# Performance work log

Hardware: AMD Instinct MI355X
Metric: run time of the kernel (lower is better)

The kernel has to match this reference:

```python
import jax, jax.numpy as jnp
import numpy as np

B, T, C = 2, 2048, 1024
H = 16
D = C // H          # head_dim = 64
WIN = 256           # local window


def _rope(x):
    # x: [B, H, T, D]; rotate pairs (even, odd) with per-pair frequencies.
    t = x.shape[2]
    d = x.shape[-1] // 2
    theta = 10000.0 ** (-(jnp.arange(d, dtype=x.dtype) / d))          # [d]
    ang = jnp.arange(t, dtype=x.dtype)[:, None] * theta               # [T, d]
    sin, cos = jnp.sin(ang), jnp.cos(ang)                             # [T, d]
    x1, x2 = x[..., ::2], x[..., 1::2]                                # [B,H,T,d]
    out = jnp.stack([x1 * cos - x2 * sin, x1 * sin + x2 * cos], axis=-1)
    return out.reshape(x.shape)


def setup_inputs() -> dict:
    key = jax.random.key(0)
    k1, k2, k3 = jax.random.split(key, 3)
    s = 1.0 / np.sqrt(C)
    return {
        "x": jax.random.normal(k1, (B, T, C), dtype=jnp.float32),
        "w_qkv": jax.random.normal(k2, (3 * C, C), dtype=jnp.float32) * s,
        "w_out": jax.random.normal(k3, (C, C), dtype=jnp.float32) * s,
        "b_out": jnp.zeros((C,), dtype=jnp.float32),
    }


def reference(x, w_qkv, w_out, b_out):
    b, t, c = x.shape
    qkv = x @ w_qkv.T                                   # [B,T,3C]
    qkv = qkv.reshape(b, t, H, 3 * D).transpose(0, 2, 1, 3)  # [B,H,T,3D]
    q, k, v = jnp.split(qkv, 3, axis=-1)                # each [B,H,T,D]
    q, k = _rope(q), _rope(k)
    scores = jnp.einsum("bhqd,bhkd->bhqk", q, k) / jnp.sqrt(jnp.asarray(D, x.dtype))
    i = jnp.arange(t)[:, None]
    j = jnp.arange(t)[None, :]
    mask = (j <= i) & (j >= i - WIN)                    # causal local window
    scores = jnp.where(mask, scores, -jnp.inf)
    attn = jax.nn.softmax(scores, axis=-1)              # [B,H,T,T]
    out = jnp.einsum("bhqk,bhkd->bhqd", attn, v)        # [B,H,T,D]
    out = out.transpose(0, 2, 1, 3).reshape(b, t, c)    # [B,T,C]
    return out @ w_out.T + b_out
```

## Files before the change

### kernel.cpp

```cpp
#include <hip/hip_runtime.h>
#include <math.h>

#define BB 2
#define TT 2048
#define CC 1024
#define HH 16
#define DD 64
#define WINW 256

constexpr int MROWS  = BB * TT;
constexpr int NQKV   = 3 * CC;
constexpr int QKV_LD = 3 * CC;

typedef unsigned short ushort_t;
typedef __attribute__((ext_vector_type(8))) short  bf16x8;
typedef __attribute__((ext_vector_type(4))) float  f32x4;
typedef __attribute__((ext_vector_type(8))) unsigned short u16x8;

__device__ __forceinline__ float bf2f(ushort_t u) {
    return __uint_as_float(((unsigned int)u) << 16);
}
__device__ __forceinline__ ushort_t f2bf(float f) {
    unsigned int u = __float_as_uint(f);
    u += 0x7fffu + ((u >> 16) & 1u);
    return (ushort_t)(u >> 16);
}

__device__ __forceinline__ void async16(void* lds, const void* g) {
    __builtin_amdgcn_global_load_lds(
        (const __attribute__((address_space(1))) unsigned int*)g,
        (__attribute__((address_space(3))) unsigned int*)lds, 16, 0, 0);
}

#define ROPE_LN 0.2878231366242557f

constexpr int NX = MROWS * CC;
constexpr int NQ = NQKV * CC;
constexpr int NO = CC * CC;

__global__ __launch_bounds__(256)
void convert_all(const float* __restrict__ x, const float* __restrict__ wq,
                 const float* __restrict__ wo, ushort_t* __restrict__ xb,
                 ushort_t* __restrict__ wqb, ushort_t* __restrict__ wob) {
    int i = (blockIdx.x * 256 + threadIdx.x) * 4;
    const float* src;
    ushort_t* dst;
    if (i < NX)           { src = x  + i;             dst = xb  + i; }
    else if (i < NX + NQ) { src = wq + (i - NX);      dst = wqb + (i - NX); }
    else                  { src = wo + (i - NX - NQ); dst = wob + (i - NX - NQ); }
    float4 v = *(const float4*)src;
    ushort4 o;
    o.x = f2bf(v.x); o.y = f2bf(v.y); o.z = f2bf(v.z); o.w = f2bf(v.w);
    *(ushort4*)dst = o;
}

__global__ __launch_bounds__(512)
void gemm1_8phase(const ushort_t* __restrict__ A, const ushort_t* __restrict__ Bw,
                  ushort_t* __restrict__ Cc) {
    constexpr int K = 1024, N = 3072, NT = 16;
    __shared__ __align__(16) ushort_t As[2][2][256 * 32];
    __shared__ __align__(16) ushort_t Bs[2][2][256 * 32];

    const int tid  = threadIdx.x;
    const int lane = tid & 63;
    const int w    = tid >> 6;
    const int wm   = w >> 2;
    const int wn   = w & 3;
    const int fr   = lane & 15;
    const int fq   = lane >> 4;

    const int nbx = NQKV / 256;
    int flat = blockIdx.y * nbx + blockIdx.x;
    flat = (flat & 7) * 24 + (flat >> 3);
    const int bm = (flat / nbx) * 256;
    const int bn = (flat % nbx) * 256;

    const int sr  = tid >> 2;
    const int dcb = tid & 3;
    const int scb = dcb ^ ((sr >> 1) & 3);

    const int cbr = fq ^ ((fr >> 1) & 3);

    f32x4 acc[8][4];
#pragma unroll
    for (int m = 0; m < 8; ++m)
#pragma unroll
        for (int n = 0; n < 4; ++n)
            acc[m][n] = f32x4{0.f, 0.f, 0.f, 0.f};

#pragma unroll
    for (int p = 0; p < 4; ++p) {
        const int skh = p >> 1;
        const bool isB = p & 1;
        const ushort_t* G = isB ? Bw : A;
        const int br = isB ? bn : bm;
        ushort_t* L = isB ? &Bs[0][skh][0] : &As[0][skh][0];
#pragma unroll
        for (int hh = 0; hh < 2; ++hh)
            async16(&L[(hh * 128 + sr) * 32 + dcb * 8],
                    G + (size_t)(br + hh * 128 + sr) * K + skh * 32 + scb * 8);
    }

    for (int t = 0; t < NT; ++t) {
        const int d  = t & 1;
        const int tn = (t + 1) & (NT - 1);
        bf16x8 bfr[4];

#pragma unroll
        for (int ph = 0; ph < 4; ++ph) {
            const int kh = ph >> 1;
            const int mh = ph & 1;

            {
                const int skh = ph >> 1;
                const bool isB = ph & 1;
                const ushort_t* G = isB ? Bw : A;
                const int br = isB ? bn : bm;
                ushort_t* L = isB ? &Bs[d ^ 1][skh][0] : &As[d ^ 1][skh][0];
#pragma unroll
                for (int hh = 0; hh < 2; ++hh)
                    async16(&L[(hh * 128 + sr) * 32 + dcb * 8],
                            G + (size_t)(br + hh * 128 + sr) * K
                              + (size_t)tn * 64 + skh * 32 + scb * 8);
            }

            if (mh == 0)
                asm volatile("s_waitcnt vmcnt(6)" ::: "memory");
            __builtin_amdgcn_s_barrier();
            __builtin_amdgcn_sched_barrier(0);

            if (mh == 0) {
#pragma unroll
                for (int n = 0; n < 4; ++n) {
                    const int rb = wn * 64 + n * 16 + fr;
                    bfr[n] = *(const bf16x8*)&Bs[d][kh][rb * 32 + cbr * 8];
                }
            }
            bf16x8 afr[4];
#pragma unroll
            for (int i = 0; i < 4; ++i) {
                const int ra = wm * 128 + (mh * 4 + i) * 16 + fr;
                afr[i] = *(const bf16x8*)&As[d][kh][ra * 32 + cbr * 8];
            }

            __builtin_amdgcn_s_setprio(1);
#pragma unroll
            for (int i = 0; i < 4; ++i)
#pragma unroll
                for (int n = 0; n < 4; ++n)
                    acc[mh * 4 + i][n] = __builtin_amdgcn_mfma_f32_16x16x32_bf16(
                        afr[i], bfr[n], acc[mh * 4 + i][n], 0, 0, 0);
            __builtin_amdgcn_s_setprio(0);
            __builtin_amdgcn_s_barrier();
        }
    }

    asm volatile("s_waitcnt vmcnt(0)" ::: "memory");

#pragma unroll
    for (int m = 0; m < 8; ++m)
#pragma unroll
        for (int n = 0; n < 4; ++n)
#pragma unroll
            for (int j = 0; j < 4; ++j) {
                const int row = bm + wm * 128 + m * 16 + fq * 4 + j;
                const int col = bn + wn * 64 + n * 16 + fr;
                Cc[(size_t)row * N + col] = f2bf(acc[m][n][j]);
            }
}

template <bool BIAS, bool OUT_BF16>
__global__ __launch_bounds__(256)
void gemm_nt_mfma(const ushort_t* __restrict__ A, const ushort_t* __restrict__ Bw,
                  const float* __restrict__ bias, void* __restrict__ Cc,
                  int M, int N, int K) {
    __shared__ __align__(16) ushort_t As[128 * 32];
    __shared__ __align__(16) ushort_t Bs[128 * 32];

    const int tid  = threadIdx.x;
    const int lane = tid & 63;
    const int wv   = tid >> 6;
    const int wr   = wv >> 1;
    const int wc   = wv & 1;

    const int nbx = gridDim.x;
    const int nwg = nbx * gridDim.y;
    int flat = blockIdx.y * nbx + blockIdx.x;
    flat = (flat & 7) * (nwg >> 3) + (flat >> 3);
    const int bm = (flat / nbx) * 128;
    const int bn = (flat % nbx) * 128;

    const int srow = tid >> 2;
    const int scol = (tid & 3) * 8;

    const ushort_t* Ag = A + (size_t)(bm + srow) * K + scol;
    const ushort_t* Bg = Bw + (size_t)(bn + srow) * K + scol;

    f32x4 acc[4][4];
#pragma unroll
    for (int m = 0; m < 4; ++m)
#pragma unroll
        for (int n = 0; n < 4; ++n)
            acc[m][n] = f32x4{0.f, 0.f, 0.f, 0.f};

    const int fr = lane & 15;
    const int fq = lane >> 4;

    for (int k0 = 0; k0 < K; k0 += 32) {
        async16(&As[tid * 8],        Ag);
        async16(&As[2048 + tid * 8], Ag + (size_t)64 * K);
        async16(&Bs[tid * 8],        Bg);
        async16(&Bs[2048 + tid * 8], Bg + (size_t)64 * K);
        Ag += 32; Bg += 32;
        __syncthreads();

        bf16x8 af[4], bfv[4];
#pragma unroll
        for (int m = 0; m < 4; ++m)
            af[m] = *(const bf16x8*)&As[(wr * 64 + m * 16 + fr) * 32 + fq * 8];
#pragma unroll
        for (int n = 0; n < 4; ++n)
            bfv[n] = *(const bf16x8*)&Bs[(wc * 64 + n * 16 + fr) * 32 + fq * 8];
#pragma unroll
        for (int m = 0; m < 4; ++m)
#pragma unroll
            for (int n = 0; n < 4; ++n)
                acc[m][n] = __builtin_amdgcn_mfma_f32_16x16x32_bf16(
                    af[m], bfv[n], acc[m][n], 0, 0, 0);
        __syncthreads();
    }

#pragma unroll
    for (int m = 0; m < 4; ++m) {
#pragma unroll
        for (int n = 0; n < 4; ++n) {
            const int col = bn + wc * 64 + n * 16 + fr;
            const float bv = BIAS ? bias[col] : 0.0f;
#pragma unroll
            for (int j = 0; j < 4; ++j) {
                const int row = bm + wr * 64 + m * 16 + fq * 4 + j;
                float v = acc[m][n][j] + bv;
                if (OUT_BF16)
                    ((ushort_t*)Cc)[(size_t)row * N + col] = f2bf(v);
                else
                    ((float*)Cc)[(size_t)row * N + col] = v;
            }
        }
    }
}

#define MASKNEG (-1e30f)

__global__ __launch_bounds__(512)
void attn_mfma(const ushort_t* __restrict__ qkv, ushort_t* __restrict__ out) {
    __shared__ __align__(16) ushort_t Ks[2][64 * 64];
    __shared__ __align__(16) ushort_t Vt[2][64 * 74];
    __shared__ __align__(16) ushort_t Ps[8][16 * 72];

    const int tid  = threadIdx.x;
    const int lane = tid & 63;
    const int w    = tid >> 6;
    const int fr   = lane & 15;
    const int fq   = lane >> 4;

    const int blk = blockIdx.x;
    const int qt  = blk & 15;
    const int h   = (blk >> 4) & 15;
    const int b   = blk >> 8;
    const int q0  = qt * 128;

    const ushort_t* base = qkv + (size_t)(b * TT) * QKV_LD + h * (3 * DD);

    const int srow = tid >> 3;
    const int dcb  = tid & 7;
    const int cbs  = dcb ^ (srow & 7);

    float thK[4];
#pragma unroll
    for (int e = 0; e < 4; ++e)
        thK[e] = __expf(-ROPE_LN * (float)(cbs * 4 + e));

    bf16x8 qf0, qf1;
    {
        const int tq = q0 + w * 16 + fr;
        const ushort_t* qrow = base + (size_t)tq * QKV_LD;
        u16x8 r0 = *(const u16x8*)(qrow + fq * 8);
        u16x8 r1 = *(const u16x8*)(qrow + 32 + fq * 8);
        const float tf = (float)tq;
#pragma unroll
        for (int e = 0; e < 4; ++e) {
            float th0 = __expf(-ROPE_LN * (float)(fq * 4 + e));
            float a0 = tf * th0;
            float s0 = __sinf(a0), c0 = __cosf(a0);
            float x1 = bf2f(r0[2 * e]), x2 = bf2f(r0[2 * e + 1]);
            r0[2 * e]     = f2bf(x1 * c0 - x2 * s0);
            r0[2 * e + 1] = f2bf(x1 * s0 + x2 * c0);
            float th1 = __expf(-ROPE_LN * (float)(16 + fq * 4 + e));
            float a1 = tf * th1;
            float s1 = __sinf(a1), c1 = __cosf(a1);
            float y1 = bf2f(r1[2 * e]), y2 = bf2f(r1[2 * e + 1]);
            r1[2 * e]     = f2bf(y1 * c1 - y2 * s1);
            r1[2 * e + 1] = f2bf(y1 * s1 + y2 * c1);
        }
        qf0 = *(bf16x8*)&r0;
        qf1 = *(bf16x8*)&r1;
    }

    f32x4 oacc[4];
#pragma unroll
    for (int nd = 0; nd < 4; ++nd) oacc[nd] = f32x4{0.f, 0.f, 0.f, 0.f};
    float mj[4], lj[4];
#pragma unroll
    for (int j = 0; j < 4; ++j) { mj[j] = MASKNEG; lj[j] = 0.f; }

    const int kstart = (q0 >= WINW) ? (q0 - WINW) : 0;
    const int ntiles = (q0 + 128 - kstart) >> 6;
    const int qlo = q0 + w * 16;

    {
        const ushort_t* rowp = base + (size_t)(kstart + srow) * QKV_LD;
        u16x8 kv = *(const u16x8*)(rowp + DD + cbs * 8);
        u16x8 vv = *(const u16x8*)(rowp + 2 * DD + dcb * 8);
        const float tf = (float)(kstart + srow);
#pragma unroll
        for (int e = 0; e < 4; ++e) {
            float a = tf * thK[e];
            float s = __sinf(a), c = __cosf(a);
            float x1 = bf2f(kv[2 * e]), x2 = bf2f(kv[2 * e + 1]);
            kv[2 * e]     = f2bf(x1 * c - x2 * s);
            kv[2 * e + 1] = f2bf(x1 * s + x2 * c);
        }
        *(u16x8*)&Ks[0][tid * 8] = kv;
#pragma unroll
        for (int e = 0; e < 8; ++e)
            Vt[0][(dcb * 8 + e) * 74 + srow] = vv[e];
    }
    __syncthreads();

    int cur = 0;
    for (int t = 0; t < ntiles; ++t) {
        const int kt0 = kstart + t * 64;
        const bool pf = (t + 1 < ntiles);
        const bool act = (kt0 <= qlo + 15) && (kt0 + 63 >= qlo - WINW);

        u16x8 kpre, vpre;
        if (pf) {
            const ushort_t* rowp = base + (size_t)(kt0 + 64 + srow) * QKV_LD;
            kpre = *(const u16x8*)(rowp + DD + cbs * 8);
            vpre = *(const u16x8*)(rowp + 2 * DD + dcb * 8);
        }

        if (act) {
            f32x4 s[4];
#pragma unroll
            for (int n = 0; n < 4; ++n) {
                const int krow = n * 16 + fr;
                bf16x8 kb0 = *(const bf16x8*)&Ks[cur][krow * 64 + ((fq ^ (krow & 7)) * 8)];
                bf16x8 kb1 = *(const bf16x8*)&Ks[cur][krow * 64 + (((fq + 4) ^ (krow & 7)) * 8)];
                f32x4 z = f32x4{0.f, 0.f, 0.f, 0.f};
                z = __builtin_amdgcn_mfma_f32_16x16x32_bf16(qf0, kb0, z, 0, 0, 0);
                s[n] = __builtin_amdgcn_mfma_f32_16x16x32_bf16(qf1, kb1, z, 0, 0, 0);
            }

            float pmax[4];
#pragma unroll
            for (int j = 0; j < 4; ++j) pmax[j] = MASKNEG;
#pragma unroll
            for (int n = 0; n < 4; ++n) {
                const int key = kt0 + n * 16 + fr;
#pragma unroll
                for (int j = 0; j < 4; ++j) {
                    const int qi = qlo + fq * 4 + j;
                    const bool ok = (key <= qi) && (key >= qi - WINW);
                    float sv = ok ? s[n][j] * 0.125f : MASKNEG;
                    s[n][j] = sv;
                    pmax[j] = fmaxf(pmax[j], sv);
                }
            }
#pragma unroll
            for (int off = 1; off < 16; off <<= 1)
#pragma unroll
                for (int j = 0; j < 4; ++j)
                    pmax[j] = fmaxf(pmax[j], __shfl_xor(pmax[j], off));

            float tl[4] = {0.f, 0.f, 0.f, 0.f};
#pragma unroll
            for (int j = 0; j < 4; ++j) {
                float mnew = fmaxf(mj[j], pmax[j]);
                float alpha = (mnew <= -1e29f) ? 1.0f : __expf(mj[j] - mnew);
                mj[j] = mnew;
                lj[j] *= alpha;
#pragma unroll
                for (int nd = 0; nd < 4; ++nd) oacc[nd][j] *= alpha;
            }
#pragma unroll
            for (int n = 0; n < 4; ++n) {
#pragma unroll
                for (int j = 0; j < 4; ++j) {
                    float sv = s[n][j];
                    float p = (sv <= -1e29f) ? 0.f : __expf(sv - mj[j]);
                    tl[j] += p;
                    Ps[w][(fq * 4 + j) * 72 + n * 16 + fr] = f2bf(p);
                }
            }
#pragma unroll
            for (int off = 1; off < 16; off <<= 1)
#pragma unroll
                for (int j = 0; j < 4; ++j)
                    tl[j] += __shfl_xor(tl[j], off);
#pragma unroll
            for (int j = 0; j < 4; ++j) lj[j] += tl[j];
        }

        if (pf) {
            const float tf = (float)(kt0 + 64 + srow);
#pragma unroll
            for (int e = 0; e < 4; ++e) {
                float a = tf * thK[e];
                float s2 = __sinf(a), c2 = __cosf(a);
                float x1 = bf2f(kpre[2 * e]), x2 = bf2f(kpre[2 * e + 1]);
                kpre[2 * e]     = f2bf(x1 * c2 - x2 * s2);
                kpre[2 * e + 1] = f2bf(x1 * s2 + x2 * c2);
            }
            *(u16x8*)&Ks[cur ^ 1][tid * 8] = kpre;
#pragma unroll
            for (int e = 0; e < 8; ++e)
                Vt[cur ^ 1][(dcb * 8 + e) * 74 + srow] = vpre[e];
        }

        if (act) {
            bf16x8 pa0 = *(const bf16x8*)&Ps[w][fr * 72 + fq * 8];
            bf16x8 pa1 = *(const bf16x8*)&Ps[w][fr * 72 + 32 + fq * 8];
#pragma unroll
            for (int nd = 0; nd < 4; ++nd) {
                bf16x8 vb0 = *(const bf16x8*)&Vt[cur][(nd * 16 + fr) * 74 + fq * 8];
                bf16x8 vb1 = *(const bf16x8*)&Vt[cur][(nd * 16 + fr) * 74 + 32 + fq * 8];
                oacc[nd] = __builtin_amdgcn_mfma_f32_16x16x32_bf16(pa0, vb0, oacc[nd], 0, 0, 0);
                oacc[nd] = __builtin_amdgcn_mfma_f32_16x16x32_bf16(pa1, vb1, oacc[nd], 0, 0, 0);
            }
        }

        __syncthreads();
        cur ^= 1;
    }

#pragma unroll
    for (int nd = 0; nd < 4; ++nd) {
#pragma unroll
        for (int j = 0; j < 4; ++j) {
            const int qi = qlo + fq * 4 + j;
            out[(size_t)(b * TT + qi) * CC + h * DD + nd * 16 + fr] =
                f2bf(oacc[nd][j] / lj[j]);
        }
    }
}

extern "C" void kernel_launch(void* const* d_in, const int* in_sizes, int n_in,
                              void* d_out, int out_size, void* d_ws, size_t ws_size,
                              hipStream_t stream) {
    const float* x     = (const float*)d_in[0];
    const float* w_qkv = (const float*)d_in[1];
    const float* w_out = (const float*)d_in[2];
    const float* b_out = (const float*)d_in[3];
    float* out = (float*)d_out;

    ushort_t* qkv_b  = (ushort_t*)d_ws;
    ushort_t* attn_b = qkv_b  + (size_t)MROWS * NQKV;
    ushort_t* xb     = attn_b + (size_t)MROWS * CC;
    ushort_t* wqb    = xb     + (size_t)MROWS * CC;
    ushort_t* wob    = wqb    + (size_t)NQKV * CC;

    convert_all<<<(NX + NQ + NO) / 1024, 256, 0, stream>>>(
        x, w_qkv, w_out, xb, wqb, wob);

    gemm1_8phase<<<dim3(NQKV / 256, MROWS / 256), 512, 0, stream>>>(
        xb, wqb, qkv_b);

    attn_mfma<<<BB * HH * (TT / 128), 512, 0, stream>>>(qkv_b, attn_b);

    gemm_nt_mfma<true, false><<<dim3(CC / 128, MROWS / 128), 256, 0, stream>>>(
        attn_b, wob, b_out, out, MROWS, CC, CC);
}
```

Before: 104.0 us.

## Use 256x192 tiles in QKV GEMM to fill all CUs

Shrinks the QKV projection GEMM's N tile from 256 to 192 columns, raising the grid from 12x16=192 to 16x16=256 workgroups so it matches the 256 CUs on MI355X and avoids a partial wave. The B tile layout becomes a single 192x64 LDS buffer with an 8-way XOR swizzle, and the async load schedule and vmcnt wait are reworked to match. Each block does less work per A load, so data reuse per tile drops a little.

```diff
diff --git a/kernel.cpp b/kernel.cpp
--- a/kernel.cpp
+++ b/kernel.cpp
@@ -58,8 +58,9 @@
 void gemm1_8phase(const ushort_t* __restrict__ A, const ushort_t* __restrict__ Bw,
                   ushort_t* __restrict__ Cc) {
     constexpr int K = 1024, N = 3072, NT = 16;
+    constexpr int BN = 192;
     __shared__ __align__(16) ushort_t As[2][2][256 * 32];
-    __shared__ __align__(16) ushort_t Bs[2][2][256 * 32];
+    __shared__ __align__(16) ushort_t Bs[2][192 * 64];
 
     const int tid  = threadIdx.x;
     const int lane = tid & 63;
@@ -69,85 +70,96 @@
     const int fr   = lane & 15;
     const int fq   = lane >> 4;
 
-    const int nbx = NQKV / 256;
-    int flat = blockIdx.y * nbx + blockIdx.x;
-    flat = (flat & 7) * 24 + (flat >> 3);
-    const int bm = (flat / nbx) * 256;
-    const int bn = (flat % nbx) * 256;
-
-    const int sr  = tid >> 2;
-    const int dcb = tid & 3;
-    const int scb = dcb ^ ((sr >> 1) & 3);
-
-    const int cbr = fq ^ ((fr >> 1) & 3);
-
-    f32x4 acc[8][4];
+    int flat = blockIdx.y * 16 + blockIdx.x;
+    flat = (flat & 7) * 32 + (flat >> 3);
+    const int bm = (flat >> 4) * 256;
+    const int bn = (flat & 15) * BN;
+
+    const int srA  = tid >> 2;
+    const int dcbA = tid & 3;
+    const int scbA = dcbA ^ ((srA >> 1) & 3);
+
+    const int srB  = tid >> 3;
+    const int dcbB = tid & 7;
+    const int scbB = dcbB ^ ((srB >> 1) & 7);
+
+    const int cbrA = fq ^ ((fr >> 1) & 3);
+
+    f32x4 acc[8][3];
 #pragma unroll
     for (int m = 0; m < 8; ++m)
 #pragma unroll
-        for (int n = 0; n < 4; ++n)
+        for (int n = 0; n < 3; ++n)
             acc[m][n] = f32x4{0.f, 0.f, 0.f, 0.f};
 
 #pragma unroll
-    for (int p = 0; p < 4; ++p) {
-        const int skh = p >> 1;
-        const bool isB = p & 1;
-        const ushort_t* G = isB ? Bw : A;
-        const int br = isB ? bn : bm;
-        ushort_t* L = isB ? &Bs[0][skh][0] : &As[0][skh][0];
-#pragma unroll
-        for (int hh = 0; hh < 2; ++hh)
-            async16(&L[(hh * 128 + sr) * 32 + dcb * 8],
-                    G + (size_t)(br + hh * 128 + sr) * K + skh * 32 + scb * 8);
-    }
+    for (int hh = 0; hh < 2; ++hh)
+        async16(&As[0][0][hh * 4096 + tid * 8],
+                A + (size_t)(bm + hh * 128 + srA) * K + scbA * 8);
+#pragma unroll
+    for (int j = 0; j < 3; ++j)
+        async16(&Bs[0][j * 4096 + tid * 8],
+                Bw + (size_t)(bn + j * 64 + srB) * K + scbB * 8);
+#pragma unroll
+    for (int hh = 0; hh < 2; ++hh)
+        async16(&As[0][1][hh * 4096 + tid * 8],
+                A + (size_t)(bm + hh * 128 + srA) * K + 32 + scbA * 8);
 
     for (int t = 0; t < NT; ++t) {
         const int d  = t & 1;
         const int tn = (t + 1) & (NT - 1);
-        bf16x8 bfr[4];
+        bf16x8 bfr[3];
 
 #pragma unroll
         for (int ph = 0; ph < 4; ++ph) {
             const int kh = ph >> 1;
             const int mh = ph & 1;
 
-            {
-                const int skh = ph >> 1;
-                const bool isB = ph & 1;
-                const ushort_t* G = isB ? Bw : A;
-                const int br = isB ? bn : bm;
-                ushort_t* L = isB ? &Bs[d ^ 1][skh][0] : &As[d ^ 1][skh][0];
+            if (ph == 0) {
 #pragma unroll
                 for (int hh = 0; hh < 2; ++hh)
-                    async16(&L[(hh * 128 + sr) * 32 + dcb * 8],
-                            G + (size_t)(br + hh * 128 + sr) * K
-                              + (size_t)tn * 64 + skh * 32 + scb * 8);
-            }
-
-            if (mh == 0)
-                asm volatile("s_waitcnt vmcnt(6)" ::: "memory");
+                    async16(&As[d ^ 1][0][hh * 4096 + tid * 8],
+                            A + (size_t)(bm + hh * 128 + srA) * K
+                              + (size_t)tn * 64 + scbA * 8);
+            } else if (ph == 1) {
+#pragma unroll
+                for (int j = 0; j < 3; ++j)
+                    async16(&Bs[d ^ 1][j * 4096 + tid * 8],
+                            Bw + (size_t)(bn + j * 64 + srB) * K
+                               + (size_t)tn * 64 + scbB * 8);
+            } else if (ph == 2) {
+#pragma unroll
+                for (int hh = 0; hh < 2; ++hh)
+                    async16(&As[d ^ 1][1][hh * 4096 + tid * 8],
+                            A + (size_t)(bm + hh * 128 + srA) * K
+                              + (size_t)tn * 64 + 32 + scbA * 8);
+            }
+
+            if (ph == 0)
+                asm volatile("s_waitcnt vmcnt(2)" ::: "memory");
             __builtin_amdgcn_s_barrier();
             __builtin_amdgcn_sched_barrier(0);
 
             if (mh == 0) {
 #pragma unroll
-                for (int n = 0; n < 4; ++n) {
-                    const int rb = wn * 64 + n * 16 + fr;
-                    bfr[n] = *(const bf16x8*)&Bs[d][kh][rb * 32 + cbr * 8];
+                for (int n = 0; n < 3; ++n) {
+                    const int rb = wn * 48 + n * 16 + fr;
+                    const int cb = (kh * 4 + fq) ^ ((rb >> 1) & 7);
+                    bfr[n] = *(const bf16x8*)&Bs[d][rb * 64 + cb * 8];
                 }
             }
             bf16x8 afr[4];
 #pragma unroll
             for (int i = 0; i < 4; ++i) {
                 const int ra = wm * 128 + (mh * 4 + i) * 16 + fr;
-                afr[i] = *(const bf16x8*)&As[d][kh][ra * 32 + cbr * 8];
+                afr[i] = *(const bf16x8*)&As[d][kh][ra * 32 + cbrA * 8];
             }
 
             __builtin_amdgcn_s_setprio(1);
 #pragma unroll
             for (int i = 0; i < 4; ++i)
 #pragma unroll
-                for (int n = 0; n < 4; ++n)
+                for (int n = 0; n < 3; ++n)
                     acc[mh * 4 + i][n] = __builtin_amdgcn_mfma_f32_16x16x32_bf16(
                         afr[i], bfr[n], acc[mh * 4 + i][n], 0, 0, 0);
             __builtin_amdgcn_s_setprio(0);
@@ -160,11 +172,11 @@
 #pragma unroll
     for (int m = 0; m < 8; ++m)
 #pragma unroll
-        for (int n = 0; n < 4; ++n)
+        for (int n = 0; n < 3; ++n)
 #pragma unroll
             for (int j = 0; j < 4; ++j) {
                 const int row = bm + wm * 128 + m * 16 + fq * 4 + j;
-                const int col = bn + wn * 64 + n * 16 + fr;
+                const int col = bn + wn * 48 + n * 16 + fr;
                 Cc[(size_t)row * N + col] = f2bf(acc[m][n][j]);
             }
 }
@@ -473,7 +485,7 @@
     convert_all<<<(NX + NQ + NO) / 1024, 256, 0, stream>>>(
         x, w_qkv, w_out, xb, wqb, wob);
 
-    gemm1_8phase<<<dim3(NQKV / 256, MROWS / 256), 512, 0, stream>>>(
+    gemm1_8phase<<<dim3(NQKV / 192, MROWS / 256), 512, 0, stream>>>(
         xb, wqb, qkv_b);
 
     attn_mfma<<<BB * HH * (TT / 128), 512, 0, stream>>>(qkv_b, attn_b);
```

Result: no change. 106.0 us (+2.0%).
